# Optimization experiments

Measured on AMD Instinct MI355X. Metric: run time of the kernel, lower is better.

The kernel has to match this reference:

```python
import jax, jax.numpy as jnp
import numpy as np

N = 50000        # number of nodes
E = 1600000      # number of (directed) edges, ~degree 32
D = 128          # latent_dim
L = 2            # num_layers
NEG_SLOPE = 0.01 # torch F.leaky_relu default


def setup_inputs() -> dict:
    key = jax.random.key(0)
    k1, k2, k3, k4 = jax.random.split(key, 4)
    h = jax.random.normal(k1, (N, D), dtype=jnp.float32)
    src = jax.random.randint(k2, (E,), 0, N, dtype=jnp.int32)
    dst = jax.random.randint(k3, (E,), 0, N, dtype=jnp.int32)
    # attn_fc per layer: Linear(2*D, 1, bias=False) -> weight vector of length 2*D
    att_w = jax.random.normal(k4, (L, 2 * D), dtype=jnp.float32) * 0.1
    return {"h": h, "src": src, "dst": dst, "att_w": att_w}


def _segment_softmax(e, seg, n):
    # numerically-stable softmax over edges grouped by destination node
    m = jax.ops.segment_max(e, seg, num_segments=n)      # [N]
    ex = jnp.exp(e - m[seg])                             # [E]
    s = jax.ops.segment_sum(ex, seg, num_segments=n)     # [N]
    return ex / s[seg]


def reference(h, src, dst, att_w):
    n, d = h.shape
    for l in range(att_w.shape[0]):
        w_src = att_w[l, :d]   # weight applied to edges.src['h']
        w_dst = att_w[l, d:]   # weight applied to edges.dst['h']
        # a = attn_fc(concat(h_src, h_dst)) = h_src @ w_src + h_dst @ w_dst
        a = h[src] @ w_src + h[dst] @ w_dst               # [E]
        e = jnp.where(a > 0, a, NEG_SLOPE * a)            # leaky_relu
        alpha = _segment_softmax(e, dst, n)               # edge_softmax by dst
        # update_all: m = h_src * e ; h_dst = sum(m)
        h = jax.ops.segment_sum(h[src] * alpha[:, None], dst, num_segments=n)
    return h
```

## Files before the change

### kernel.cpp

```cpp
#include <hip/hip_runtime.h>
#include <hip/hip_fp16.h>
#include <math.h>

#define NEG_SLOPE 0.01f
#define BKT_BITS 7
#define BKT_MASK 127
#define SBLOCKS  256
#define STPB     512


__global__ void bkhist_kernel(const int* __restrict__ dst, int* __restrict__ blockhist,
                              int E, int NB, int chunk) {
    extern __shared__ int lh[];
    for (int k = threadIdx.x; k < NB; k += blockDim.x) lh[k] = 0;
    __syncthreads();
    int b = blockIdx.x;
    int beg = b * chunk, end = min(E, beg + chunk);
    for (int e = beg + (int)threadIdx.x; e < end; e += blockDim.x)
        atomicAdd(&lh[dst[e] >> BKT_BITS], 1);
    __syncthreads();
    for (int k = threadIdx.x; k < NB; k += blockDim.x)
        blockhist[k * SBLOCKS + b] = lh[k];
}

__global__ void scan1_kernel(const int* __restrict__ in, int* __restrict__ local_excl,
                             int* __restrict__ partials, int n) {
    __shared__ int sm[1024];
    int i = blockIdx.x * 1024 + threadIdx.x;
    int x = (i < n) ? in[i] : 0;
    sm[threadIdx.x] = x;
    __syncthreads();
    for (int off = 1; off < 1024; off <<= 1) {
        int y = (threadIdx.x >= (unsigned)off) ? sm[threadIdx.x - off] : 0;
        __syncthreads();
        sm[threadIdx.x] += y;
        __syncthreads();
    }
    if (i < n) local_excl[i] = sm[threadIdx.x] - x;
    if (threadIdx.x == 1023) partials[blockIdx.x] = sm[1023];
}

__global__ void scan2_kernel(int* __restrict__ partials, int nchunks) {
    __shared__ int sm[1024];
    int x = (threadIdx.x < (unsigned)nchunks) ? partials[threadIdx.x] : 0;
    sm[threadIdx.x] = x;
    __syncthreads();
    for (int off = 1; off < 1024; off <<= 1) {
        int y = (threadIdx.x >= (unsigned)off) ? sm[threadIdx.x - off] : 0;
        __syncthreads();
        sm[threadIdx.x] += y;
        __syncthreads();
    }
    partials[threadIdx.x] = sm[threadIdx.x] - x;
    if (threadIdx.x == 1023) partials[1024] = sm[1023];
}

__global__ void scan3_kernel(const int* __restrict__ local_excl, const int* __restrict__ partials,
                             int* __restrict__ out, int n) {
    int i = blockIdx.x * 1024 + threadIdx.x;
    if (i < n) out[i] = local_excl[i] + partials[blockIdx.x];
    if (i == n) out[n] = partials[1024];
}

__global__ void bksplit_kernel(const int* __restrict__ src, const int* __restrict__ dst,
                               const int* __restrict__ bh_scan, unsigned* __restrict__ pairs,
                               int E, int NB, int chunk) {
    extern __shared__ int lm[];
    int* lbase = lm;
    int* lcnt  = lm + NB;
    int b = blockIdx.x;
    for (int k = threadIdx.x; k < NB; k += blockDim.x) {
        lbase[k] = bh_scan[k * SBLOCKS + b];
        lcnt[k]  = 0;
    }
    __syncthreads();
    int beg = b * chunk, end = min(E, beg + chunk);
    for (int e = beg + (int)threadIdx.x; e < end; e += blockDim.x) {
        int d = dst[e];
        int k = d >> BKT_BITS;
        int pos = lbase[k] + atomicAdd(&lcnt[k], 1);
        pairs[pos] = ((unsigned)src[e] << BKT_BITS) | (unsigned)(d & BKT_MASK);
    }
}

__global__ void csr_build_kernel(const unsigned* __restrict__ pairs, const int* __restrict__ bh_scan,
                                 int* __restrict__ row_ptr, int* __restrict__ csr_src,
                                 int E, int N, int NB) {
    __shared__ int ldeg[128];
    __shared__ int lscan[128];
    __shared__ int lpos[128];
    int k = blockIdx.x;
    int bbase = bh_scan[k * SBLOCKS];
    int bend  = bh_scan[(k + 1) * SBLOCKS];
    if (threadIdx.x < 128) ldeg[threadIdx.x] = 0;
    __syncthreads();
    for (int i = bbase + (int)threadIdx.x; i < bend; i += blockDim.x)
        atomicAdd(&ldeg[pairs[i] & BKT_MASK], 1);
    __syncthreads();
    int x = (threadIdx.x < 128) ? ldeg[threadIdx.x] : 0;
    if (threadIdx.x < 128) lscan[threadIdx.x] = x;
    __syncthreads();
    for (int off = 1; off < 128; off <<= 1) {
        int y = 0;
        if (threadIdx.x < 128 && threadIdx.x >= (unsigned)off) y = lscan[threadIdx.x - off];
        __syncthreads();
        if (threadIdx.x < 128) lscan[threadIdx.x] += y;
        __syncthreads();
    }
    if (threadIdx.x < 128) {
        int excl = lscan[threadIdx.x] - x;
        int node = (k << BKT_BITS) + threadIdx.x;
        if (node < N) row_ptr[node] = bbase + excl;
        lpos[threadIdx.x] = excl;
    }
    if (k == NB - 1 && threadIdx.x == 0) row_ptr[N] = E;
    __syncthreads();
    for (int i = bbase + (int)threadIdx.x; i < bend; i += blockDim.x) {
        unsigned p = pairs[i];
        int pos = atomicAdd(&lpos[p & BKT_MASK], 1);
        csr_src[bbase + pos] = (int)(p >> BKT_BITS);
    }
}


__global__ void stconv_kernel(const float* __restrict__ h, const float* __restrict__ att_w_l,
                              float* __restrict__ s, float* __restrict__ t,
                              __half* __restrict__ h16, int n) {
    int gid  = blockIdx.x * blockDim.x + threadIdx.x;
    int wid  = gid >> 6;
    int lane = threadIdx.x & 63;
    int half = lane >> 5;
    int hl   = lane & 31;
    int v    = wid * 2 + half;
    if (v >= n) return;
    float4 hv = ((const float4*)(h + (size_t)v * 128))[hl];
    __half2 p01 = __floats2half2_rn(hv.x, hv.y);
    __half2 p23 = __floats2half2_rn(hv.z, hv.w);
    float2 packed;
    packed.x = *(const float*)&p01;
    packed.y = *(const float*)&p23;
    ((float2*)(h16 + (size_t)v * 128))[hl] = packed;
    float4 ws = ((const float4*)att_w_l)[hl];
    float4 wd = ((const float4*)(att_w_l + 128))[hl];
    float ps = hv.x * ws.x + hv.y * ws.y + hv.z * ws.z + hv.w * ws.w;
    float pt = hv.x * wd.x + hv.y * wd.y + hv.z * wd.z + hv.w * wd.w;
    for (int off = 16; off > 0; off >>= 1) {
        ps += __shfl_down(ps, off);
        pt += __shfl_down(pt, off);
    }
    if (hl == 0) { s[v] = ps; t[v] = pt; }
}

__device__ __forceinline__ void gath8(const __half* __restrict__ hin, int u, float w,
                                      int qlane, float acc[8]) {
    float4 r = ((const float4*)(hin + (size_t)u * 128))[qlane];
    const __half2* hp = (const __half2*)&r;
    float2 f0 = __half22float2(hp[0]);
    float2 f1 = __half22float2(hp[1]);
    float2 f2 = __half22float2(hp[2]);
    float2 f3 = __half22float2(hp[3]);
    acc[0] = fmaf(w, f0.x, acc[0]); acc[1] = fmaf(w, f0.y, acc[1]);
    acc[2] = fmaf(w, f1.x, acc[2]); acc[3] = fmaf(w, f1.y, acc[3]);
    acc[4] = fmaf(w, f2.x, acc[4]); acc[5] = fmaf(w, f2.y, acc[5]);
    acc[6] = fmaf(w, f3.x, acc[6]); acc[7] = fmaf(w, f3.y, acc[7]);
}

template<bool LAST>
__global__ void agg_kernel(const __half* __restrict__ hin, const float* __restrict__ s,
                           const float* __restrict__ t, const int* __restrict__ row_ptr,
                           const int* __restrict__ csr_src,
                           __half* __restrict__ hout16, float* __restrict__ outf,
                           const float* __restrict__ att_w_next,
                           float* __restrict__ s2, float* __restrict__ t2, int n) {
    int gid   = blockIdx.x * blockDim.x + threadIdx.x;
    int v     = gid >> 6;
    int lane  = threadIdx.x & 63;
    if (v >= n) return;
    int quad  = lane >> 4;
    int qlane = lane & 15;

    int beg = row_ptr[v];
    int end = row_ptr[v + 1];
    float tv = t[v];

    float acc[8] = {0.f, 0.f, 0.f, 0.f, 0.f, 0.f, 0.f, 0.f};
    float lsum_l = 0.f;

    for (int base = beg; base < end; base += 64) {
        int cnt = end - base;
        if (cnt > 64) cnt = 64;
        int idx = base + min(lane, cnt - 1);
        int u   = csr_src[idx];
        float a = s[u] + tv;
        float e = (a > 0.f) ? a : NEG_SLOPE * a;
        float wl = (lane < cnt) ? __expf(e) : 0.f;
        lsum_l += wl;
        int steps = (cnt + 3) >> 2;
        int k = 0;
        for (; k + 3 < steps; k += 4) {
            int sl0 = (k << 2) + quad;
            int   u0 = __shfl(u, sl0);       float w0 = __shfl(wl, sl0);
            int   u1 = __shfl(u, sl0 + 4);   float w1 = __shfl(wl, sl0 + 4);
            int   u2 = __shfl(u, sl0 + 8);   float w2 = __shfl(wl, sl0 + 8);
            int   u3 = __shfl(u, sl0 + 12);  float w3 = __shfl(wl, sl0 + 12);
            gath8(hin, u0, w0, qlane, acc);
            gath8(hin, u1, w1, qlane, acc);
            gath8(hin, u2, w2, qlane, acc);
            gath8(hin, u3, w3, qlane, acc);
        }
        for (; k < steps; ++k) {
            int sl = (k << 2) + quad;
            int   u0 = __shfl(u, sl);
            float w0 = __shfl(wl, sl);
            gath8(hin, u0, w0, qlane, acc);
        }
    }
    #pragma unroll
    for (int j = 0; j < 8; ++j) {
        acc[j] += __shfl_xor(acc[j], 16);
        acc[j] += __shfl_xor(acc[j], 32);
    }
    float lsum = lsum_l;
    for (int off = 32; off > 0; off >>= 1) lsum += __shfl_xor(lsum, off);
    float inv_l = (lsum > 0.f) ? (1.0f / lsum) : 0.f;
    #pragma unroll
    for (int j = 0; j < 8; ++j) acc[j] *= inv_l;

    if (LAST) {
        if (quad == 0) {
            float4* op = (float4*)(outf + (size_t)v * 128);
            op[2 * qlane]     = make_float4(acc[0], acc[1], acc[2], acc[3]);
            op[2 * qlane + 1] = make_float4(acc[4], acc[5], acc[6], acc[7]);
        }
    } else {
        if (quad == 0) {
            __half2 p0 = __floats2half2_rn(acc[0], acc[1]);
            __half2 p1 = __floats2half2_rn(acc[2], acc[3]);
            __half2 p2 = __floats2half2_rn(acc[4], acc[5]);
            __half2 p3 = __floats2half2_rn(acc[6], acc[7]);
            int4 pk;
            pk.x = *(const int*)&p0; pk.y = *(const int*)&p1;
            pk.z = *(const int*)&p2; pk.w = *(const int*)&p3;
            ((int4*)(hout16 + (size_t)v * 128))[qlane] = pk;
        }
        float4 ws0 = ((const float4*)att_w_next)[2 * qlane];
        float4 ws1 = ((const float4*)att_w_next)[2 * qlane + 1];
        float4 wd0 = ((const float4*)(att_w_next + 128))[2 * qlane];
        float4 wd1 = ((const float4*)(att_w_next + 128))[2 * qlane + 1];
        float ps = acc[0] * ws0.x + acc[1] * ws0.y + acc[2] * ws0.z + acc[3] * ws0.w
                 + acc[4] * ws1.x + acc[5] * ws1.y + acc[6] * ws1.z + acc[7] * ws1.w;
        float pt = acc[0] * wd0.x + acc[1] * wd0.y + acc[2] * wd0.z + acc[3] * wd0.w
                 + acc[4] * wd1.x + acc[5] * wd1.y + acc[6] * wd1.z + acc[7] * wd1.w;
        for (int off = 8; off > 0; off >>= 1) {
            ps += __shfl_down(ps, off);
            pt += __shfl_down(pt, off);
        }
        if (lane == 0) { s2[v] = ps; t2[v] = pt; }
    }
}


extern "C" void kernel_launch(void* const* d_in, const int* in_sizes, int n_in,
                              void* d_out, int out_size, void* d_ws, size_t ws_size,
                              hipStream_t stream) {
    const float* h0    = (const float*)d_in[0];
    const int*   src   = (const int*)d_in[1];
    const int*   dst   = (const int*)d_in[2];
    const float* att_w = (const float*)d_in[3];
    int N = in_sizes[0] / 128;
    int E = in_sizes[1];
    int L = in_sizes[3] / 256;
    float* out = (float*)d_out;

    int NB = (N + BKT_MASK) >> BKT_BITS;
    int n2 = NB * SBLOCKS;
    int chunk = (E + SBLOCKS - 1) / SBLOCKS;
    int nch2 = (n2 + 1023) / 1024;

    char* ws = (char*)d_ws;
    size_t off = 0;
    auto alloc = [&](size_t bytes) -> void* {
        void* p = ws + off;
        off = (off + bytes + 511) & ~(size_t)511;
        return p;
    };
    int*      row_ptr   = (int*)     alloc((size_t)(N + 1) * 4);
    int*      csr_src   = (int*)     alloc((size_t)E * 4);
    float*    s1        = (float*)   alloc((size_t)N * 4);
    float*    t1        = (float*)   alloc((size_t)N * 4);
    float*    s2        = (float*)   alloc((size_t)N * 4);
    float*    t2        = (float*)   alloc((size_t)N * 4);
    __half*   hA        = (__half*)  alloc((size_t)N * 128 * 2);
    __half*   hB        = (__half*)  alloc((size_t)N * 128 * 2);
    unsigned* pairs     = (unsigned*)alloc((size_t)E * 4);
    int*      blockhist = (int*)     alloc((size_t)n2 * 4);
    int*      bh_scan   = (int*)     alloc((size_t)(n2 + 1) * 4);
    int*      local_ex  = (int*)     alloc((size_t)n2 * 4);
    int*      partials  = (int*)     alloc(1025 * 4);

    bkhist_kernel<<<SBLOCKS, STPB, NB * 4, stream>>>(dst, blockhist, E, NB, chunk);
    scan1_kernel<<<nch2, 1024, 0, stream>>>(blockhist, local_ex, partials, n2);
    scan2_kernel<<<1, 1024, 0, stream>>>(partials, nch2);
    scan3_kernel<<<nch2, 1024, 0, stream>>>(local_ex, partials, bh_scan, n2);
    bksplit_kernel<<<SBLOCKS, STPB, 2 * NB * 4, stream>>>(src, dst, bh_scan, pairs, E, NB, chunk);
    csr_build_kernel<<<NB, 512, 0, stream>>>(pairs, bh_scan, row_ptr, csr_src, E, N, NB);

    const int tb = 256;
    int node_blocks = (N * 64 + tb - 1) / tb;
    int st_blocks   = ((N + 1) / 2 * 64 + tb - 1) / tb;

    stconv_kernel<<<st_blocks, tb, 0, stream>>>(h0, att_w, s1, t1, hA, N);

    __half* hin = hA;
    __half* hnx = hB;
    float *sc = s1, *tc = t1, *sn = s2, *tn = t2;
    for (int l = 0; l < L; ++l) {
        if (l == L - 1) {
            agg_kernel<true><<<node_blocks, tb, 0, stream>>>(
                hin, sc, tc, row_ptr, csr_src, nullptr, out, nullptr, nullptr, nullptr, N);
        } else {
            agg_kernel<false><<<node_blocks, tb, 0, stream>>>(
                hin, sc, tc, row_ptr, csr_src, hnx, nullptr,
                att_w + (size_t)(l + 1) * 256, sn, tn, N);
            __half* tmp = hin; hin = hnx; hnx = tmp;
            float* tf;
            tf = sc; sc = sn; sn = tf;
            tf = tc; tc = tn; tn = tf;
        }
    }
}
```

Measured before the change: 220.8 us.

## Fold scan3 into consumers and batch 8 gathers before FMAs in aggregation

Drops the scan3 kernel launch: the bucket-histogram consumers now add the per-chunk partial to the local exclusive scan inline, and the last bucket's end is taken as E. Separately, the aggregation inner loop is unrolled to 8 neighbor rows, with all 8 shuffles and 8 row loads issued before any FMA, so more gather loads are in flight per wave. The cost is higher register pressure from holding eight float4 rows, which may reduce occupancy.

```diff
diff --git a/kernel.cpp b/kernel.cpp
--- a/kernel.cpp
+++ b/kernel.cpp
@@ -55,22 +55,21 @@
     if (threadIdx.x == 1023) partials[1024] = sm[1023];
 }
 
-__global__ void scan3_kernel(const int* __restrict__ local_excl, const int* __restrict__ partials,
-                             int* __restrict__ out, int n) {
-    int i = blockIdx.x * 1024 + threadIdx.x;
-    if (i < n) out[i] = local_excl[i] + partials[blockIdx.x];
-    if (i == n) out[n] = partials[1024];
+__device__ __forceinline__ int bh_at(const int* __restrict__ local_ex,
+                                     const int* __restrict__ partials, int i) {
+    return local_ex[i] + partials[i >> 10];
 }
 
 __global__ void bksplit_kernel(const int* __restrict__ src, const int* __restrict__ dst,
-                               const int* __restrict__ bh_scan, unsigned* __restrict__ pairs,
+                               const int* __restrict__ local_ex, const int* __restrict__ partials,
+                               unsigned* __restrict__ pairs,
                                int E, int NB, int chunk) {
     extern __shared__ int lm[];
     int* lbase = lm;
     int* lcnt  = lm + NB;
     int b = blockIdx.x;
     for (int k = threadIdx.x; k < NB; k += blockDim.x) {
-        lbase[k] = bh_scan[k * SBLOCKS + b];
+        lbase[k] = bh_at(local_ex, partials, k * SBLOCKS + b);
         lcnt[k]  = 0;
     }
     __syncthreads();
@@ -83,15 +82,16 @@
     }
 }
 
-__global__ void csr_build_kernel(const unsigned* __restrict__ pairs, const int* __restrict__ bh_scan,
+__global__ void csr_build_kernel(const unsigned* __restrict__ pairs,
+                                 const int* __restrict__ local_ex, const int* __restrict__ partials,
                                  int* __restrict__ row_ptr, int* __restrict__ csr_src,
                                  int E, int N, int NB) {
     __shared__ int ldeg[128];
     __shared__ int lscan[128];
     __shared__ int lpos[128];
     int k = blockIdx.x;
-    int bbase = bh_scan[k * SBLOCKS];
-    int bend  = bh_scan[(k + 1) * SBLOCKS];
+    int bbase = bh_at(local_ex, partials, k * SBLOCKS);
+    int bend  = (k == NB - 1) ? E : bh_at(local_ex, partials, (k + 1) * SBLOCKS);
     if (threadIdx.x < 128) ldeg[threadIdx.x] = 0;
     __syncthreads();
     for (int i = bbase + (int)threadIdx.x; i < bend; i += blockDim.x)
@@ -151,18 +151,13 @@
     if (hl == 0) { s[v] = ps; t[v] = pt; }
 }
 
-__device__ __forceinline__ void gath8(const __half* __restrict__ hin, int u, float w,
-                                      int qlane, float acc[8]) {
-    float4 r = ((const float4*)(hin + (size_t)u * 128))[qlane];
+__device__ __forceinline__ void fma_row(const float4& r, float w, float acc[8]) {
     const __half2* hp = (const __half2*)&r;
-    float2 f0 = __half22float2(hp[0]);
-    float2 f1 = __half22float2(hp[1]);
-    float2 f2 = __half22float2(hp[2]);
-    float2 f3 = __half22float2(hp[3]);
-    acc[0] = fmaf(w, f0.x, acc[0]); acc[1] = fmaf(w, f0.y, acc[1]);
-    acc[2] = fmaf(w, f1.x, acc[2]); acc[3] = fmaf(w, f1.y, acc[3]);
-    acc[4] = fmaf(w, f2.x, acc[4]); acc[5] = fmaf(w, f2.y, acc[5]);
-    acc[6] = fmaf(w, f3.x, acc[6]); acc[7] = fmaf(w, f3.y, acc[7]);
+    #pragma unroll
+    for (int d = 0; d < 4; ++d) {
+        acc[2 * d]     = fmaf(__low2float(hp[d]),  w, acc[2 * d]);
+        acc[2 * d + 1] = fmaf(__high2float(hp[d]), w, acc[2 * d + 1]);
+    }
 }
 
 template<bool LAST>
@@ -197,22 +192,29 @@
         lsum_l += wl;
         int steps = (cnt + 3) >> 2;
         int k = 0;
-        for (; k + 3 < steps; k += 4) {
-            int sl0 = (k << 2) + quad;
-            int   u0 = __shfl(u, sl0);       float w0 = __shfl(wl, sl0);
-            int   u1 = __shfl(u, sl0 + 4);   float w1 = __shfl(wl, sl0 + 4);
-            int   u2 = __shfl(u, sl0 + 8);   float w2 = __shfl(wl, sl0 + 8);
-            int   u3 = __shfl(u, sl0 + 12);  float w3 = __shfl(wl, sl0 + 12);
-            gath8(hin, u0, w0, qlane, acc);
-            gath8(hin, u1, w1, qlane, acc);
-            gath8(hin, u2, w2, qlane, acc);
-            gath8(hin, u3, w3, qlane, acc);
+        for (; k + 8 <= steps; k += 8) {
+            int   uu[8];
+            float ww[8];
+            #pragma unroll
+            for (int j = 0; j < 8; ++j) {
+                int sl = ((k + j) << 2) + quad;
+                uu[j] = __shfl(u, sl);
+                ww[j] = __shfl(wl, sl);
+            }
+            float4 rr[8];
+            #pragma unroll
+            for (int j = 0; j < 8; ++j)
+                rr[j] = ((const float4*)(hin + ((size_t)(unsigned)uu[j] << 7)))[qlane];
+            #pragma unroll
+            for (int j = 0; j < 8; ++j)
+                fma_row(rr[j], ww[j], acc);
         }
         for (; k < steps; ++k) {
             int sl = (k << 2) + quad;
             int   u0 = __shfl(u, sl);
             float w0 = __shfl(wl, sl);
-            gath8(hin, u0, w0, qlane, acc);
+            float4 r = ((const float4*)(hin + ((size_t)(unsigned)u0 << 7)))[qlane];
+            fma_row(r, w0, acc);
         }
     }
     #pragma unroll
@@ -294,16 +296,16 @@
     __half*   hB        = (__half*)  alloc((size_t)N * 128 * 2);
     unsigned* pairs     = (unsigned*)alloc((size_t)E * 4);
     int*      blockhist = (int*)     alloc((size_t)n2 * 4);
-    int*      bh_scan   = (int*)     alloc((size_t)(n2 + 1) * 4);
     int*      local_ex  = (int*)     alloc((size_t)n2 * 4);
     int*      partials  = (int*)     alloc(1025 * 4);
 
     bkhist_kernel<<<SBLOCKS, STPB, NB * 4, stream>>>(dst, blockhist, E, NB, chunk);
     scan1_kernel<<<nch2, 1024, 0, stream>>>(blockhist, local_ex, partials, n2);
     scan2_kernel<<<1, 1024, 0, stream>>>(partials, nch2);
-    scan3_kernel<<<nch2, 1024, 0, stream>>>(local_ex, partials, bh_scan, n2);
-    bksplit_kernel<<<SBLOCKS, STPB, 2 * NB * 4, stream>>>(src, dst, bh_scan, pairs, E, NB, chunk);
-    csr_build_kernel<<<NB, 512, 0, stream>>>(pairs, bh_scan, row_ptr, csr_src, E, N, NB);
+    bksplit_kernel<<<SBLOCKS, STPB, 2 * NB * 4, stream>>>(src, dst, local_ex, partials,
+                                                          pairs, E, NB, chunk);
+    csr_build_kernel<<<NB, 512, 0, stream>>>(pairs, local_ex, partials,
+                                             row_ptr, csr_src, E, N, NB);
 
     const int tb = 256;
     int node_blocks = (N * 64 + tb - 1) / tb;
```

Result: slower. 236.7 us (+7.2%).
